# Optimization experiments

Hardware: AMD Instinct MI355X
Metric: run time of the kernel (lower is better)

## Reference

```python
import jax, jax.numpy as jnp
import numpy as np

B, T, EMB, HS = 4, 4096, 1024, 64
BASE = 10000.0


def rope_angles(T, hs, base=BASE):
    # theta_i = base^(-2i/hs), freqs[t, i] = t * theta_i  -> (T, hs//2)
    inv = 1.0 / (base ** (2.0 * jnp.arange(hs // 2, dtype=jnp.float32) / hs))
    return jnp.arange(T, dtype=jnp.float32)[:, None] * inv[None, :]


def apply_rope(x, cos, sin):
    # x: (B, T, D); pairs are interleaved (even, odd) like torch.view_as_complex
    xr = x.reshape(*x.shape[:-1], -1, 2)
    xe, xo = xr[..., 0], xr[..., 1]
    re = xe * cos - xo * sin
    im = xe * sin + xo * cos
    return jnp.stack([re, im], axis=-1).reshape(x.shape)


def setup_inputs() -> dict:
    key = jax.random.key(0)
    kx, kq, kk, kv = jax.random.split(key, 4)
    s = 1.0 / np.sqrt(EMB)
    return {
        "x": jax.random.normal(kx, (B, T, EMB), jnp.float32),
        "Wq": jax.random.normal(kq, (HS, EMB), jnp.float32) * s,
        "Wk": jax.random.normal(kk, (HS, EMB), jnp.float32) * s,
        "Wv": jax.random.normal(kv, (HS, EMB), jnp.float32) * s,
    }


def reference(x, Wq, Wk, Wv):
    Tlen = x.shape[1]
    ang = rope_angles(Tlen, HS)          # (T, HS//2)
    cos, sin = jnp.cos(ang), jnp.sin(ang)
    q = x @ Wq.T                          # (B, T, HS)
    k = x @ Wk.T
    v = x @ Wv.T
    q = apply_rope(q, cos, sin)
    k = apply_rope(k, cos, sin)
    scores = jnp.einsum("bqd,bkd->bqk", q, k) * (HS ** -0.5)
    causal = jnp.tril(jnp.ones((Tlen, Tlen), dtype=bool))
    scores = jnp.where(causal[None], scores, -jnp.inf)
    w = jax.nn.softmax(scores, axis=-1)   # dropout in eval mode: identity
    return jnp.einsum("bqk,bkd->bqd", w, v)
```

## Files before the change

### kernel.cpp

```cpp
#include <hip/hip_runtime.h>

typedef __bf16 bf16x8 __attribute__((ext_vector_type(8)));
typedef __bf16 bf16x4 __attribute__((ext_vector_type(4)));
typedef float f32x4 __attribute__((ext_vector_type(4)));
typedef float f32x16 __attribute__((ext_vector_type(16)));
typedef unsigned int u32;

#define T_LEN 4096

__device__ __forceinline__ f32x4 mfma16(bf16x8 a, bf16x8 b, f32x4 c) {
    return __builtin_amdgcn_mfma_f32_16x16x32_bf16(a, b, c, 0, 0, 0);
}
__device__ __forceinline__ f32x16 mfma32(bf16x8 a, bf16x8 b, f32x16 c) {
    return __builtin_amdgcn_mfma_f32_32x32x16_bf16(a, b, c, 0, 0, 0);
}
__device__ __forceinline__ u32 packbf(float lo, float hi) {
    union { __bf16 e[2]; u32 w; } u;
    u.e[0] = (__bf16)lo; u.e[1] = (__bf16)hi;
    return u.w;
}
__device__ __forceinline__ f32x16 zero16() {
    f32x16 z;
    #pragma unroll
    for (int i = 0; i < 16; i++) z[i] = 0.f;
    return z;
}
__device__ __forceinline__ void gload_lds16(const __bf16* g, __bf16* l) {
    __builtin_amdgcn_global_load_lds(
        (const __attribute__((address_space(1))) u32*)g,
        (__attribute__((address_space(3))) u32*)l, 16, 0, 0);
}

__global__ __launch_bounds__(256) void convert_w_kernel(
    const float* __restrict__ Wq, const float* __restrict__ Wk,
    const float* __restrict__ Wv, __bf16* __restrict__ wf)
{
    int t = blockIdx.x * 256 + threadIdx.x;
    int ks = t / 1536;
    int rem = t - ks * 1536;
    int n = rem >> 3, g = rem & 7;
    const float* src = (n < 64 ? Wq : (n < 128 ? Wk : Wv))
                     + (size_t)(n & 63) * 1024 + ks * 64 + g * 8;
    float4 f0 = *(const float4*)src;
    float4 f1 = *(const float4*)(src + 4);
    bf16x8 h = {(__bf16)f0.x, (__bf16)f0.y, (__bf16)f0.z, (__bf16)f0.w,
                (__bf16)f1.x, (__bf16)f1.y, (__bf16)f1.z, (__bf16)f1.w};
    int chunk = n * 8 + (g ^ (n & 7));
    *(bf16x8*)(wf + (size_t)ks * 12288 + chunk * 8) = h;
}

__global__ __launch_bounds__(512, 2) void proj_kernel(
    const float* __restrict__ x, const __bf16* __restrict__ wf,
    __bf16* __restrict__ qfb, __bf16* __restrict__ kfb, __bf16* __restrict__ vfb)
{
    __shared__ __bf16 smem[33792];
    __bf16 (*xs)[64][72] = (__bf16(*)[64][72])smem;
    __bf16* wl = smem + 9216;
    __bf16* stage = smem;

    const int tid  = threadIdx.x;
    const int wave = tid >> 6, lane = tid & 63;
    const int l15 = lane & 15, l4 = lane >> 4;
    const int wm = wave >> 2, wn = wave & 3;
    const size_t m0 = (size_t)blockIdx.x * 64;
    const int srow = tid >> 3, scp = (tid & 7) * 8;

    f32x4 acc[2][3];
    #pragma unroll
    for (int a = 0; a < 2; a++)
        #pragma unroll
        for (int bn = 0; bn < 3; bn++) acc[a][bn] = (f32x4){0.f, 0.f, 0.f, 0.f};

    const float* xsrc = x + (m0 + srow) * 1024 + scp;

    float4 rx0, rx1;

    rx0 = *(const float4*)(xsrc);
    rx1 = *(const float4*)(xsrc + 4);
    {
        bf16x8 h = {(__bf16)rx0.x, (__bf16)rx0.y, (__bf16)rx0.z, (__bf16)rx0.w,
                    (__bf16)rx1.x, (__bf16)rx1.y, (__bf16)rx1.z, (__bf16)rx1.w};
        *(bf16x8*)&xs[0][srow][scp] = h;
        __bf16* wdst = wl + wave * 512;
        #pragma unroll
        for (int i = 0; i < 3; i++)
            gload_lds16(wf + (size_t)i * 4096 + (size_t)tid * 8, wdst + i * 4096);
    }
    __syncthreads();

    for (int t = 0; t < 16; t++) {
        const int cur = t & 1;
        if (t < 15) {
            const int k0 = (t + 1) * 64;
            rx0 = *(const float4*)(xsrc + k0);
            rx1 = *(const float4*)(xsrc + k0 + 4);
            const __bf16* wsrc = wf + (size_t)(t + 1) * 12288;
            __bf16* wdst = wl + (cur ^ 1) * 12288 + wave * 512;
            #pragma unroll
            for (int i = 0; i < 3; i++)
                gload_lds16(wsrc + (size_t)i * 4096 + (size_t)tid * 8, wdst + i * 4096);
        }
        const __bf16* wcur = wl + cur * 12288;
        bf16x8 af[2][2];
        #pragma unroll
        for (int mf = 0; mf < 2; mf++)
            #pragma unroll
            for (int c = 0; c < 2; c++)
                af[mf][c] = *(const bf16x8*)&xs[cur][wm * 32 + mf * 16 + l15][c * 32 + l4 * 8];
        #pragma unroll
        for (int nf = 0; nf < 3; nf++) {
            const int n = wn * 48 + nf * 16 + l15;
            const int sw = n & 7;
            #pragma unroll
            for (int c = 0; c < 2; c++) {
                bf16x8 bw = *(const bf16x8*)(wcur + (size_t)(n * 8 + ((c * 4 + l4) ^ sw)) * 8);
                #pragma unroll
                for (int mf = 0; mf < 2; mf++)
                    acc[mf][nf] = mfma16(af[mf][c], bw, acc[mf][nf]);
            }
        }
        if (t < 15) {
            bf16x8 h = {(__bf16)rx0.x, (__bf16)rx0.y, (__bf16)rx0.z, (__bf16)rx0.w,
                        (__bf16)rx1.x, (__bf16)rx1.y, (__bf16)rx1.z, (__bf16)rx1.w};
            *(bf16x8*)&xs[cur ^ 1][srow][scp] = h;
        }
        __syncthreads();
    }

    const int tq0 = (int)(m0 & 4095);
    #pragma unroll
    for (int nf = 0; nf < 3; nf++) {
        int n = wn * 48 + nf * 16 + l15;
        #pragma unroll
        for (int mf = 0; mf < 2; mf++) {
            #pragma unroll
            for (int r = 0; r < 4; r++) {
                int row64 = wm * 32 + mf * 16 + l4 * 4 + r;
                int tile = row64 >> 5, rr = row64 & 31;
                int tb = tile * 6144;
                float val = acc[mf][nf][r];
                float partner = __shfl_xor(val, 1);
                if (n < 128) {
                    int i = (n & 63) >> 1;
                    float ang = (float)(tq0 + row64)
                              * __builtin_exp2f((float)i * (-13.287712379549449f / 32.f));
                    float sn, cs;
                    __sincosf(ang, &sn, &cs);
                    float res = (n & 1) ? (partner * sn + val * cs)
                                        : (val * cs - partner * sn);
                    if (n < 64) {
                        res *= 0.180336884f;
                        int d = n;
                        stage[tb + (d >> 4) * 512
                              + (rr + ((d >> 3) & 1) * 32) * 8 + (d & 7)] = (__bf16)res;
                    } else {
                        int d = n - 64;
                        int l31i = ((rr >> 2) & 1) * 16 + ((rr >> 4) & 1) * 8
                                 + ((rr >> 3) & 1) * 4 + (rr & 3);
                        stage[tb + 2048 + (d >> 4) * 512
                              + (l31i + ((d >> 3) & 1) * 32) * 8 + (d & 7)] = (__bf16)res;
                    }
                } else {
                    int d = n - 128;
                    int cc = ((d >> 5) << 1) | (rr >> 4);
                    stage[tb + 4096 + cc * 512
                          + ((d & 31) + ((rr >> 3) & 1) * 32) * 8 + (rr & 7)]
                        = (__bf16)val;
                }
            }
        }
    }
    __syncthreads();
    {
        const size_t bbase = (size_t)(m0 >> 12) * 262144;
        const size_t tbase = (size_t)((m0 & 4095) >> 5) * 2048;
        #pragma unroll
        for (int tile = 0; tile < 2; tile++) {
            const int tb = tile * 6144;
            const size_t go = bbase + tbase + (size_t)tile * 2048 + tid * 4;
            bf16x4 q4 = *(const bf16x4*)&stage[tb + tid * 4];
            bf16x4 k4 = *(const bf16x4*)&stage[tb + 2048 + tid * 4];
            bf16x4 v4 = *(const bf16x4*)&stage[tb + 4096 + tid * 4];
            *(bf16x4*)(qfb + go) = q4;
            *(bf16x4*)(kfb + go) = k4;
            *(bf16x4*)(vfb + go) = v4;
        }
    }
}

__global__ __launch_bounds__(1024) void flash_kernel(
    const __bf16* __restrict__ qfb, const __bf16* __restrict__ kfb,
    const __bf16* __restrict__ vfb, float* __restrict__ out)
{
    __shared__ float ods[16][32][36];
    __shared__ float mls[2][16][32];

    const int tid = threadIdx.x;
    const int wave = tid >> 6, lane = tid & 63;
    const int l31 = lane & 31, h = lane >> 5;
    const int xcd = blockIdx.x & 7;
    const int b = xcd >> 1;
    const int p = ((blockIdx.x >> 3) << 1) | (xcd & 1);

    const __bf16* qb_b = qfb + (size_t)b * 262144;
    const __bf16* kb_b = kfb + (size_t)b * 262144;
    const __bf16* vb_b = vfb + (size_t)b * 262144;

    #pragma unroll 1
    for (int half = 0; half < 2; half++) {
        const int jt = half ? p : 127 - p;
        const int q0 = jt * 32;
        const int qg = q0 + l31;

        const __bf16* qp = qb_b + (size_t)jt * 2048 + lane * 8;
        bf16x8 qf[4];
        #pragma unroll
        for (int dc = 0; dc < 4; dc++) qf[dc] = *(const bf16x8*)(qp + dc * 512);

        float m = 16.f, l = 0.f;
        f32x16 o0 = zero16(), o1 = zero16();
        const int nt = jt + 1;

        #pragma unroll 1
        for (int kt = wave; kt < nt; kt += 16) {
            const int kc0 = kt << 5;
            const __bf16* kr = kb_b + (size_t)kt * 2048 + lane * 8;
            bf16x8 kf0 = *(const bf16x8*)(kr);
            bf16x8 kf1 = *(const bf16x8*)(kr + 512);
            bf16x8 kf2 = *(const bf16x8*)(kr + 1024);
            bf16x8 kf3 = *(const bf16x8*)(kr + 1536);
            const __bf16* vr = vb_b + (size_t)kt * 2048 + lane * 8;
            bf16x8 vf00 = *(const bf16x8*)(vr);
            bf16x8 vf01 = *(const bf16x8*)(vr + 512);
            bf16x8 vf10 = *(const bf16x8*)(vr + 1024);
            bf16x8 vf11 = *(const bf16x8*)(vr + 1536);
            f32x16 s = zero16();
            __builtin_amdgcn_s_setprio(1);
            s = mfma32(kf0, qf[0], s);
            s = mfma32(kf1, qf[1], s);
            s = mfma32(kf2, qf[2], s);
            s = mfma32(kf3, qf[3], s);
            __builtin_amdgcn_s_setprio(0);
            if (kt == jt) {
                #pragma unroll
                for (int r = 0; r < 16; r++) {
                    int pioff = ((r >> 2) & 1) * 16 + 8 * h + (r >> 3) * 4 + (r & 3);
                    if (kc0 + pioff > qg) s[r] = -1e30f;
                }
            }
            float tm[8];
            #pragma unroll
            for (int i = 0; i < 8; i++) tm[i] = fmaxf(s[2 * i], s[2 * i + 1]);
            #pragma unroll
            for (int i = 0; i < 4; i++) tm[i] = fmaxf(tm[i], tm[i + 4]);
            float tmax = fmaxf(fmaxf(tm[0], tm[1]), fmaxf(tm[2], tm[3]));
            float ts[4] = {0.f, 0.f, 0.f, 0.f};
            #pragma unroll
            for (int r = 0; r < 16; r++) {
                float e = __builtin_exp2f(s[r] - m);
                s[r] = e;
                ts[r & 3] += e;
            }
            float lsum = (ts[0] + ts[1]) + (ts[2] + ts[3]);
            float lsum_p = __shfl_xor(lsum, 32);
            float tmax_p = __shfl_xor(tmax, 32);
            union { u32 w[4]; bf16x8 v; } pf[2];
            #pragma unroll
            for (int cg = 0; cg < 2; cg++) {
                pf[cg].w[0] = packbf(s[4 * cg + 0],  s[4 * cg + 1]);
                pf[cg].w[1] = packbf(s[4 * cg + 2],  s[4 * cg + 3]);
                pf[cg].w[2] = packbf(s[4 * cg + 8],  s[4 * cg + 9]);
                pf[cg].w[3] = packbf(s[4 * cg + 10], s[4 * cg + 11]);
            }
            __builtin_amdgcn_s_setprio(1);
            o0 = mfma32(vf00, pf[0].v, o0);
            o0 = mfma32(vf01, pf[1].v, o0);
            o1 = mfma32(vf10, pf[0].v, o1);
            o1 = mfma32(vf11, pf[1].v, o1);
            __builtin_amdgcn_s_setprio(0);
            l += lsum + lsum_p;
            float tmx = fmaxf(tmax, tmax_p);
            if (!__all(tmx <= m + 8.f)) {
                const float mnew = fmaxf(m, tmx);
                const float alpha = __builtin_exp2f(m - mnew);
                m = mnew;
                l *= alpha;
                #pragma unroll
                for (int r = 0; r < 16; r++) { o0[r] *= alpha; o1[r] *= alpha; }
            }
        }

        const int q = tid >> 5, dcm = tid & 31;
        #pragma unroll
        for (int c2 = 0; c2 < 4; c2++) {
            f32x4 w0 = {o0[4 * c2], o0[4 * c2 + 1], o0[4 * c2 + 2], o0[4 * c2 + 3]};
            *(f32x4*)&ods[wave][l31][8 * c2 + 4 * h] = w0;
        }
        if (h == 0) {
            mls[0][wave][l31] = (wave < nt) ? m : -1e30f;
            mls[1][wave][l31] = l;
        }
        __syncthreads();
        float M = -1e30f;
        #pragma unroll
        for (int s2 = 0; s2 < 16; s2++) M = fmaxf(M, mls[0][s2][q]);
        float w16[16], L = 0.f;
        #pragma unroll
        for (int s2 = 0; s2 < 16; s2++) {
            float ws = __builtin_exp2f(mls[0][s2][q] - M);
            w16[s2] = ws;
            L += ws * mls[1][s2][q];
        }
        const float invL = 1.f / L;
        float accA = 0.f;
        #pragma unroll
        for (int s2 = 0; s2 < 16; s2++) accA += w16[s2] * ods[s2][q][dcm];
        out[((size_t)b * T_LEN + q0 + q) * 64 + dcm] = accA * invL;
        __syncthreads();
        #pragma unroll
        for (int c2 = 0; c2 < 4; c2++) {
            f32x4 w1 = {o1[4 * c2], o1[4 * c2 + 1], o1[4 * c2 + 2], o1[4 * c2 + 3]};
            *(f32x4*)&ods[wave][l31][8 * c2 + 4 * h] = w1;
        }
        __syncthreads();
        float accB = 0.f;
        #pragma unroll
        for (int s2 = 0; s2 < 16; s2++) accB += w16[s2] * ods[s2][q][dcm];
        out[((size_t)b * T_LEN + q0 + q) * 64 + 32 + dcm] = accB * invL;
        __syncthreads();
    }
}

extern "C" void kernel_launch(void* const* d_in, const int* in_sizes, int n_in,
                              void* d_out, int out_size, void* d_ws, size_t ws_size,
                              hipStream_t stream)
{
    const float* x  = (const float*)d_in[0];
    const float* Wq = (const float*)d_in[1];
    const float* Wk = (const float*)d_in[2];
    const float* Wv = (const float*)d_in[3];
    float* out = (float*)d_out;

    __bf16* qfb = (__bf16*)d_ws;
    __bf16* kfb = qfb + 1048576;
    __bf16* vfb = kfb + 1048576;
    __bf16* wf  = vfb + 1048576;

    convert_w_kernel<<<96, 256, 0, stream>>>(Wq, Wk, Wv, wf);
    proj_kernel<<<256, 512, 0, stream>>>(x, wf, qfb, kfb, vfb);
    flash_kernel<<<256, 1024, 0, stream>>>(qfb, kfb, vfb, out);
}
```

Measured before the change: 54.16 us.

## Split projection GEMM along K into two blocks and add reduce kernel

The projection kernel now splits the 1024-wide reduction dimension in half, launching 512 blocks instead of 256 so more CUs are busy. Each block writes fp32 partial accumulators to a workspace buffer. A new reduce kernel sums the two partials and runs the existing RoPE and bf16 epilogue. This adds an extra kernel launch and a round trip of partial sums through global memory.

```diff
diff --git a/kernel.cpp b/kernel.cpp
--- a/kernel.cpp
+++ b/kernel.cpp
@@ -51,18 +51,19 @@
 
 __global__ __launch_bounds__(512, 2) void proj_kernel(
     const float* __restrict__ x, const __bf16* __restrict__ wf,
-    __bf16* __restrict__ qfb, __bf16* __restrict__ kfb, __bf16* __restrict__ vfb)
+    float* __restrict__ pacc)
 {
     __shared__ __bf16 smem[33792];
     __bf16 (*xs)[64][72] = (__bf16(*)[64][72])smem;
     __bf16* wl = smem + 9216;
-    __bf16* stage = smem;
 
     const int tid  = threadIdx.x;
     const int wave = tid >> 6, lane = tid & 63;
     const int l15 = lane & 15, l4 = lane >> 4;
     const int wm = wave >> 2, wn = wave & 3;
-    const size_t m0 = (size_t)blockIdx.x * 64;
+    const int mt = blockIdx.x >> 1, ks = blockIdx.x & 1;
+    const size_t m0 = (size_t)mt * 64;
+    const int kb0 = ks * 512;
     const int srow = tid >> 3, scp = (tid & 7) * 8;
 
     f32x4 acc[2][3];
@@ -71,7 +72,8 @@
         #pragma unroll
         for (int bn = 0; bn < 3; bn++) acc[a][bn] = (f32x4){0.f, 0.f, 0.f, 0.f};
 
-    const float* xsrc = x + (m0 + srow) * 1024 + scp;
+    const float* xsrc = x + (m0 + srow) * 1024 + kb0 + scp;
+    const __bf16* wfb = wf + (size_t)(ks * 8) * 12288;
 
     float4 rx0, rx1;
 
@@ -84,17 +86,17 @@
         __bf16* wdst = wl + wave * 512;
         #pragma unroll
         for (int i = 0; i < 3; i++)
-            gload_lds16(wf + (size_t)i * 4096 + (size_t)tid * 8, wdst + i * 4096);
+            gload_lds16(wfb + (size_t)i * 4096 + (size_t)tid * 8, wdst + i * 4096);
     }
     __syncthreads();
 
-    for (int t = 0; t < 16; t++) {
+    for (int t = 0; t < 8; t++) {
         const int cur = t & 1;
-        if (t < 15) {
+        if (t < 7) {
             const int k0 = (t + 1) * 64;
             rx0 = *(const float4*)(xsrc + k0);
             rx1 = *(const float4*)(xsrc + k0 + 4);
-            const __bf16* wsrc = wf + (size_t)(t + 1) * 12288;
+            const __bf16* wsrc = wfb + (size_t)(t + 1) * 12288;
             __bf16* wdst = wl + (cur ^ 1) * 12288 + wave * 512;
             #pragma unroll
             for (int i = 0; i < 3; i++)
@@ -119,12 +121,49 @@
                     acc[mf][nf] = mfma16(af[mf][c], bw, acc[mf][nf]);
             }
         }
-        if (t < 15) {
+        if (t < 7) {
             bf16x8 h = {(__bf16)rx0.x, (__bf16)rx0.y, (__bf16)rx0.z, (__bf16)rx0.w,
                         (__bf16)rx1.x, (__bf16)rx1.y, (__bf16)rx1.z, (__bf16)rx1.w};
             *(bf16x8*)&xs[cur ^ 1][srow][scp] = h;
         }
         __syncthreads();
+    }
+
+    {
+        float* pb = pacc + (size_t)blockIdx.x * 12288 + tid * 4;
+        #pragma unroll
+        for (int mf = 0; mf < 2; mf++)
+            #pragma unroll
+            for (int nf = 0; nf < 3; nf++)
+                *(f32x4*)(pb + (size_t)(mf * 3 + nf) * 2048) = acc[mf][nf];
+    }
+}
+
+__global__ __launch_bounds__(512, 2) void reduce_kernel(
+    const float* __restrict__ pacc,
+    __bf16* __restrict__ qfb, __bf16* __restrict__ kfb, __bf16* __restrict__ vfb)
+{
+    __shared__ __bf16 stage[12288];
+
+    const int tid  = threadIdx.x;
+    const int wave = tid >> 6, lane = tid & 63;
+    const int l15 = lane & 15, l4 = lane >> 4;
+    const int wm = wave >> 2, wn = wave & 3;
+    const int mt = blockIdx.x;
+    const size_t m0 = (size_t)mt * 64;
+
+    f32x4 acc[2][3];
+    {
+        const float* pa = pacc + (size_t)(mt * 2) * 12288 + tid * 4;
+        const float* pb = pa + 12288;
+        #pragma unroll
+        for (int mf = 0; mf < 2; mf++)
+            #pragma unroll
+            for (int nf = 0; nf < 3; nf++) {
+                f32x4 a = *(const f32x4*)(pa + (size_t)(mf * 3 + nf) * 2048);
+                f32x4 b = *(const f32x4*)(pb + (size_t)(mf * 3 + nf) * 2048);
+                acc[mf][nf] = (f32x4){a.x + b.x, a.y + b.y, a.z + b.z, a.w + b.w};
+            }
     }
 
     const int tq0 = (int)(m0 & 4095);
@@ -345,8 +384,10 @@
     __bf16* kfb = qfb + 1048576;
     __bf16* vfb = kfb + 1048576;
     __bf16* wf  = vfb + 1048576;
+    float*  pacc = (float*)(wf + 196608);
 
     convert_w_kernel<<<96, 256, 0, stream>>>(Wq, Wk, Wv, wf);
-    proj_kernel<<<256, 512, 0, stream>>>(x, wf, qfb, kfb, vfb);
+    proj_kernel<<<512, 512, 0, stream>>>(x, wf, pacc);
+    reduce_kernel<<<256, 512, 0, stream>>>(pacc, qfb, kfb, vfb);
     flash_kernel<<<256, 1024, 0, stream>>>(qfb, kfb, vfb, out);
 }
```

New measurement: 56.56 us. +4.4%, slower.
